# Performance work log

Hardware: AMD Instinct MI355X
Metric: run time of the kernel (lower is better)

Reference implementation:

```python
import jax, jax.numpy as jnp
import numpy as np

N_DAYS, N_HOURS, N_LINKS, N_FEATS = 4, 24, 2000, 4
N_PATHS, N_ODS = 20000, 4000
EPS = 1e-12


def setup_inputs() -> dict:
    key = jax.random.key(0)
    ks = jax.random.split(key, 9)
    # X: (days, hours, links, 1 + n_features); channel 0 is free-flow travel time tt_ff
    X = jax.random.uniform(ks[0], (N_DAYS, N_HOURS, N_LINKS, N_FEATS + 1), dtype=jnp.float32) + 0.1
    # utility coefficients; signs '-' for all cost features (projected via clip to <= 0)
    theta_raw = -jax.random.uniform(ks[1], (N_FEATS,), dtype=jnp.float32)
    theta_links = 0.01 * jax.random.normal(ks[2], (N_LINKS,), dtype=jnp.float32)
    q_sqrt = jax.random.uniform(ks[3], (N_ODS,), dtype=jnp.float32) + 0.5  # q = q_sqrt**2
    log_alpha = 0.1 * jax.random.normal(ks[4], (N_LINKS,), dtype=jnp.float32)
    beta_raw = jax.random.uniform(ks[5], (N_LINKS,), dtype=jnp.float32, minval=1.0, maxval=3.0)
    k = jax.random.uniform(ks[6], (N_LINKS,), dtype=jnp.float32, minval=50.0, maxval=150.0)
    # link-path incidence D (n_links, n_paths), ~10 links per path
    D = (jax.random.uniform(ks[7], (N_LINKS, N_PATHS)) < 0.005).astype(jnp.float32)
    # OD segment id of each path (sorted, one OD per path) == sparse M structure
    od_of_path = jnp.sort(jax.random.randint(ks[8], (N_PATHS,), 0, N_ODS, dtype=jnp.int32))
    return dict(X=X, theta_raw=theta_raw, theta_links=theta_links, q_sqrt=q_sqrt,
                log_alpha=log_alpha, beta_raw=beta_raw, k=k, D=D,
                od_of_path=od_of_path, n_ods=N_ODS)


def reference(X, theta_raw, theta_links, q_sqrt, log_alpha, beta_raw, k, D, od_of_path, n_ods):
    # project_theta: all features have sign '-', so clip to (-inf, 0]
    theta = jnp.minimum(theta_raw, 0.0)
    tt_ff = X[..., 0]              # (d, h, l)
    feats = X[..., 1:]             # (d, h, l, f)
    # link utilities: einsum('ijkl,l->ijk') + theta_links
    V = jnp.einsum('dhlf,f->dhl', feats, theta) + theta_links
    # path utilities: einsum('ijk,kl->ijl') with D (links, paths)
    vf = jnp.einsum('dhl,lp->dhp', V, D)            # (d, h, p)
    vf_t = jnp.moveaxis(vf, -1, 0)                  # (p, d, h) paths leading for segment ops
    # segmented softmax over paths within each OD choice set (sparse M pattern)
    vmax = jax.lax.stop_gradient(
        jax.ops.segment_max(vf_t, od_of_path, num_segments=n_ods))   # (ods, d, h)
    ev = jnp.exp(vf_t - vmax[od_of_path])
    denom = jax.ops.segment_sum(ev, od_of_path, num_segments=n_ods)[od_of_path]
    pf = ev / denom                                  # (p, d, h) path probabilities
    # path flows: pf scaled by OD demand q = q_sqrt**2
    q = q_sqrt ** 2
    f = pf * q[od_of_path][:, None, None]            # (p, d, h)
    # link flows + relu
    x = jax.nn.relu(jnp.einsum('pdh,lp->dhl', f, D))  # (d, h, l)
    # BPR link travel times: tt_ff * (1 + alpha * (x/k)^beta)
    alpha = jnp.exp(log_alpha)
    beta = jnp.clip(beta_raw, EPS, 4.0)
    return tt_ff * (1.0 + alpha * jnp.power(x / k, beta))
```

## Files before the change

kernel.cpp:

```cpp
#include <hip/hip_runtime.h>
#include <math.h>

#define NDH 96
#define ND4 24
#define NL  2000
#define NP  20000
#define NOD 4000
#define PL_CAP 32
#define LP_CAP 150
#define LP_LDS 256

typedef unsigned short u16;
typedef unsigned int   u32;

__global__ __launch_bounds__(256) void kA(const float* __restrict__ X,
                                          const float* __restrict__ theta_raw,
                                          const float* __restrict__ theta_links,
                                          float* __restrict__ V) {
    int gid = blockIdx.x * blockDim.x + threadIdx.x;
    if (gid >= NL * NDH) return;
    int l = gid / NDH, dh = gid - l * NDH;
    float t0 = fminf(theta_raw[0], 0.f);
    float t1 = fminf(theta_raw[1], 0.f);
    float t2 = fminf(theta_raw[2], 0.f);
    float t3 = fminf(theta_raw[3], 0.f);
    const float* xp = X + ((size_t)(dh * NL + l)) * 5;
    V[gid] = theta_links[l]
           + t0 * xp[1] + t1 * xp[2] + t2 * xp[3] + t3 * xp[4];
}

__global__ __launch_bounds__(256) void kB3(const float* __restrict__ D,
                                           int* __restrict__ lc,
                                           u16* __restrict__ lp) {
    __shared__ u16 slp[LP_LDS];
    __shared__ int scnt;
    int l = blockIdx.x;
    int tid = threadIdx.x;
    if (tid == 0) scnt = 0;
    __syncthreads();
    const float4* row4 = (const float4*)(D + (size_t)l * NP);
    for (int i = tid; i < NP / 4; i += 256) {
        float4 fv = row4[i];
        u32 wv[4] = { __float_as_uint(fv.x), __float_as_uint(fv.y),
                      __float_as_uint(fv.z), __float_as_uint(fv.w) };
        if ((wv[0] | wv[1] | wv[2] | wv[3]) == 0u) continue;
        int p0 = i * 4;
#pragma unroll
        for (int k = 0; k < 4; k++) {
            if (wv[k] != 0u) {
                int s = atomicAdd(&scnt, 1);
                if (s < LP_LDS) slp[s] = (u16)(p0 + k);
            }
        }
    }
    __syncthreads();
    int c = min(scnt, LP_CAP);
    for (int j = tid; j < c; j += 256) lp[l * LP_CAP + j] = slp[j];
    if (tid == 0) lc[l] = scnt;
}

__global__ __launch_bounds__(256) void kL2(const int* __restrict__ lc,
                                           const u16* __restrict__ lp,
                                           int* __restrict__ pc,
                                           u16* __restrict__ pl) {
    int t = blockIdx.x * 256 + threadIdx.x;
    int l = t >> 8, j = t & 255;
    if (l >= NL) return;
    if (j >= min(lc[l], LP_CAP)) return;
    int p = (int)lp[l * LP_CAP + j];
    int s = atomicAdd(&pc[p], 1);
    if (s < PL_CAP) pl[p * PL_CAP + s] = (u16)l;
}

__global__ __launch_bounds__(256) void kC(const int* __restrict__ od, int* __restrict__ start) {
    int o = blockIdx.x * blockDim.x + threadIdx.x;
    if (o > NOD) return;
    int lo = 0, hi = NP;
    while (lo < hi) { int mid = (lo + hi) >> 1; if (od[mid] < o) lo = mid + 1; else hi = mid; }
    start[o] = lo;
}

__global__ __launch_bounds__(256) void kD4(const float* __restrict__ V,
                                           const int* __restrict__ pc,
                                           const u16* __restrict__ pl,
                                           float* __restrict__ vf) {
    int tid = blockIdx.x * blockDim.x + threadIdx.x;
    if (tid >= NP * ND4) return;
    int p = tid / ND4, d4 = tid - p * ND4;
    int c = min(pc[p], PL_CAP);
    const u16* plrow = pl + p * PL_CAP;
    const float4* V4 = (const float4*)V;
    float4 acc = make_float4(0.f, 0.f, 0.f, 0.f);
    for (int j0 = 0; j0 < c; j0 += 8) {
        int li[8];
#pragma unroll
        for (int t = 0; t < 8; t++) li[t] = (j0 + t < c) ? (int)plrow[j0 + t] : -1;
#pragma unroll
        for (int t = 0; t < 8; t++) {
            if (li[t] >= 0) {
                float4 v = V4[li[t] * ND4 + d4];
                acc.x += v.x; acc.y += v.y; acc.z += v.z; acc.w += v.w;
            }
        }
    }
    ((float4*)vf)[p * ND4 + d4] = acc;
}

__global__ __launch_bounds__(256) void kE4(float* __restrict__ vf,
                                           const int* __restrict__ start,
                                           const float* __restrict__ q_sqrt) {
    int tid = blockIdx.x * blockDim.x + threadIdx.x;
    if (tid >= NOD * ND4) return;
    int o = tid / ND4, d4 = tid - o * ND4;
    int a = start[o], b = start[o + 1];
    if (a >= b) return;
    float4* vf4 = (float4*)vf;
    float4 m = make_float4(-INFINITY, -INFINITY, -INFINITY, -INFINITY);
    for (int p = a; p < b; p++) {
        float4 v = vf4[p * ND4 + d4];
        m.x = fmaxf(m.x, v.x); m.y = fmaxf(m.y, v.y);
        m.z = fmaxf(m.z, v.z); m.w = fmaxf(m.w, v.w);
    }
    float4 s = make_float4(0.f, 0.f, 0.f, 0.f);
    for (int p = a; p < b; p++) {
        float4 v = vf4[p * ND4 + d4];
        s.x += expf(v.x - m.x); s.y += expf(v.y - m.y);
        s.z += expf(v.z - m.z); s.w += expf(v.w - m.w);
    }
    float q = q_sqrt[o]; float qq = q * q;
    float4 rs = make_float4(qq / s.x, qq / s.y, qq / s.z, qq / s.w);
    for (int p = a; p < b; p++) {
        float4 v = vf4[p * ND4 + d4];
        v.x = expf(v.x - m.x) * rs.x; v.y = expf(v.y - m.y) * rs.y;
        v.z = expf(v.z - m.z) * rs.z; v.w = expf(v.w - m.w) * rs.w;
        vf4[p * ND4 + d4] = v;
    }
}

__global__ __launch_bounds__(192) void kF4(const float* __restrict__ f,
                                           const int* __restrict__ lc,
                                           const u16* __restrict__ lp,
                                           const float* __restrict__ X,
                                           const float* __restrict__ log_alpha,
                                           const float* __restrict__ beta_raw,
                                           const float* __restrict__ kk,
                                           float* __restrict__ out) {
    __shared__ float4 sf[8 * ND4];
    int l  = blockIdx.x;
    int d4 = threadIdx.x % ND4;
    int jc = threadIdx.x / ND4;
    int c  = min(lc[l], LP_CAP);
    const u16* lprow = lp + l * LP_CAP;
    const float4* f4 = (const float4*)f;
    float4 acc = make_float4(0.f, 0.f, 0.f, 0.f);
    for (int j = jc; j < c; j += 8) {
        float4 v = f4[(int)lprow[j] * ND4 + d4];
        acc.x += v.x; acc.y += v.y; acc.z += v.z; acc.w += v.w;
    }
    sf[jc * ND4 + d4] = acc;
    __syncthreads();
    if (jc == 0) {
        float4 t = sf[d4];
#pragma unroll
        for (int r = 1; r < 8; r++) {
            float4 u = sf[r * ND4 + d4];
            t.x += u.x; t.y += u.y; t.z += u.z; t.w += u.w;
        }
        float alpha = expf(log_alpha[l]);
        float beta  = fminf(fmaxf(beta_raw[l], 1e-12f), 4.0f);
        float kv    = kk[l];
        float xs[4] = { t.x, t.y, t.z, t.w };
#pragma unroll
        for (int k4 = 0; k4 < 4; k4++) {
            int dh = d4 * 4 + k4;
            float xv = fmaxf(xs[k4], 0.f);
            float tt = X[((size_t)(dh * NL + l)) * 5];
            out[dh * NL + l] = tt * (1.0f + alpha * powf(xv / kv, beta));
        }
    }
}

extern "C" void kernel_launch(void* const* d_in, const int* in_sizes, int n_in,
                              void* d_out, int out_size, void* d_ws, size_t ws_size,
                              hipStream_t stream) {
    const float* X           = (const float*)d_in[0];
    const float* theta_raw   = (const float*)d_in[1];
    const float* theta_links = (const float*)d_in[2];
    const float* q_sqrt      = (const float*)d_in[3];
    const float* log_alpha   = (const float*)d_in[4];
    const float* beta_raw    = (const float*)d_in[5];
    const float* kk          = (const float*)d_in[6];
    const float* D           = (const float*)d_in[7];
    const int*   od          = (const int*)d_in[8];
    float* out = (float*)d_out;
    char* ws = (char*)d_ws;

    int*   pc    = (int*)(ws + 0);
    int*   lc    = (int*)(ws + 80000);
    int*   start = (int*)(ws + 88064);
    float* V     = (float*)(ws + 104576);
    u16*   pl    = (u16*)(ws + 872576);
    u16*   lp    = (u16*)(ws + 2152576);
    float* vf    = (float*)(ws + 2785024);

    hipMemsetAsync(pc, 0, 80000, stream);

    kA <<<(NL * NDH + 255) / 256, 256, 0, stream>>>(X, theta_raw, theta_links, V);
    kB3<<<NL, 256, 0, stream>>>(D, lc, lp);
    kL2<<<(NL * 256) / 256, 256, 0, stream>>>(lc, lp, pc, pl);
    kC <<<(NOD + 1 + 255) / 256, 256, 0, stream>>>(od, start);
    kD4<<<(NP * ND4 + 255) / 256, 256, 0, stream>>>(V, pc, pl, vf);
    kE4<<<(NOD * ND4 + 255) / 256, 256, 0, stream>>>(vf, start, q_sqrt);
    kF4<<<NL, 192, 0, stream>>>(vf, lc, lp, X, log_alpha, beta_raw, kk, out);
}
```

Baseline: 307.9 us.

## Fuse path-list build into scan kernel and path-utility gather into segmented softmax

The kernel that builds link-to-path lists now also appends each link to its paths' lists, which removes a separate launch. The path-utility gather is fused into the per-OD softmax kernel and recomputed in each of its three passes, so the intermediate vf array is never written to or read from global memory. In exchange the softmax kernel launches only 96k threads instead of 480k, and it repeats the gather three times, so per-thread latency and load imbalance across ODs of different sizes can grow.

```diff
diff --git a/kernel.cpp b/kernel.cpp
--- a/kernel.cpp
+++ b/kernel.cpp
@@ -29,9 +29,11 @@
            + t0 * xp[1] + t1 * xp[2] + t2 * xp[3] + t3 * xp[4];
 }
 
-__global__ __launch_bounds__(256) void kB3(const float* __restrict__ D,
-                                           int* __restrict__ lc,
-                                           u16* __restrict__ lp) {
+__global__ __launch_bounds__(256) void kB3L(const float* __restrict__ D,
+                                            int* __restrict__ lc,
+                                            u16* __restrict__ lp,
+                                            int* __restrict__ pc,
+                                            u16* __restrict__ pl) {
     __shared__ u16 slp[LP_LDS];
     __shared__ int scnt;
     int l = blockIdx.x;
@@ -55,21 +57,13 @@
     }
     __syncthreads();
     int c = min(scnt, LP_CAP);
-    for (int j = tid; j < c; j += 256) lp[l * LP_CAP + j] = slp[j];
+    for (int j = tid; j < c; j += 256) {
+        int p = (int)slp[j];
+        lp[l * LP_CAP + j] = (u16)p;
+        int s = atomicAdd(&pc[p], 1);
+        if (s < PL_CAP) pl[p * PL_CAP + s] = (u16)l;
+    }
     if (tid == 0) lc[l] = scnt;
-}
-
-__global__ __launch_bounds__(256) void kL2(const int* __restrict__ lc,
-                                           const u16* __restrict__ lp,
-                                           int* __restrict__ pc,
-                                           u16* __restrict__ pl) {
-    int t = blockIdx.x * 256 + threadIdx.x;
-    int l = t >> 8, j = t & 255;
-    if (l >= NL) return;
-    if (j >= min(lc[l], LP_CAP)) return;
-    int p = (int)lp[l * LP_CAP + j];
-    int s = atomicAdd(&pc[p], 1);
-    if (s < PL_CAP) pl[p * PL_CAP + s] = (u16)l;
 }
 
 __global__ __launch_bounds__(256) void kC(const int* __restrict__ od, int* __restrict__ start) {
@@ -80,60 +74,76 @@
     start[o] = lo;
 }
 
-__global__ __launch_bounds__(256) void kD4(const float* __restrict__ V,
-                                           const int* __restrict__ pc,
-                                           const u16* __restrict__ pl,
-                                           float* __restrict__ vf) {
-    int tid = blockIdx.x * blockDim.x + threadIdx.x;
-    if (tid >= NP * ND4) return;
-    int p = tid / ND4, d4 = tid - p * ND4;
-    int c = min(pc[p], PL_CAP);
-    const u16* plrow = pl + p * PL_CAP;
-    const float4* V4 = (const float4*)V;
-    float4 acc = make_float4(0.f, 0.f, 0.f, 0.f);
-    for (int j0 = 0; j0 < c; j0 += 8) {
-        int li[8];
-#pragma unroll
-        for (int t = 0; t < 8; t++) li[t] = (j0 + t < c) ? (int)plrow[j0 + t] : -1;
-#pragma unroll
-        for (int t = 0; t < 8; t++) {
-            if (li[t] >= 0) {
-                float4 v = V4[li[t] * ND4 + d4];
-                acc.x += v.x; acc.y += v.y; acc.z += v.z; acc.w += v.w;
-            }
-        }
-    }
-    ((float4*)vf)[p * ND4 + d4] = acc;
-}
-
-__global__ __launch_bounds__(256) void kE4(float* __restrict__ vf,
-                                           const int* __restrict__ start,
-                                           const float* __restrict__ q_sqrt) {
+__global__ __launch_bounds__(256) void kDE4(const float* __restrict__ V,
+                                            const int* __restrict__ start,
+                                            const int* __restrict__ pc,
+                                            const u16* __restrict__ pl,
+                                            const float* __restrict__ q_sqrt,
+                                            float* __restrict__ f) {
     int tid = blockIdx.x * blockDim.x + threadIdx.x;
     if (tid >= NOD * ND4) return;
     int o = tid / ND4, d4 = tid - o * ND4;
     int a = start[o], b = start[o + 1];
     if (a >= b) return;
-    float4* vf4 = (float4*)vf;
+    const float4* V4 = (const float4*)V;
+    float4* f4 = (float4*)f;
+
     float4 m = make_float4(-INFINITY, -INFINITY, -INFINITY, -INFINITY);
     for (int p = a; p < b; p++) {
-        float4 v = vf4[p * ND4 + d4];
-        m.x = fmaxf(m.x, v.x); m.y = fmaxf(m.y, v.y);
-        m.z = fmaxf(m.z, v.z); m.w = fmaxf(m.w, v.w);
+        int c = min(pc[p], PL_CAP);
+        const u16* pr = pl + p * PL_CAP;
+        float4 acc = make_float4(0.f, 0.f, 0.f, 0.f);
+        for (int j0 = 0; j0 < c; j0 += 8) {
+            int li[8];
+#pragma unroll
+            for (int t = 0; t < 8; t++) li[t] = (j0 + t < c) ? (int)pr[j0 + t] : -1;
+#pragma unroll
+            for (int t = 0; t < 8; t++) if (li[t] >= 0) {
+                float4 v = V4[li[t] * ND4 + d4];
+                acc.x += v.x; acc.y += v.y; acc.z += v.z; acc.w += v.w;
+            }
+        }
+        m.x = fmaxf(m.x, acc.x); m.y = fmaxf(m.y, acc.y);
+        m.z = fmaxf(m.z, acc.z); m.w = fmaxf(m.w, acc.w);
     }
     float4 s = make_float4(0.f, 0.f, 0.f, 0.f);
     for (int p = a; p < b; p++) {
-        float4 v = vf4[p * ND4 + d4];
-        s.x += expf(v.x - m.x); s.y += expf(v.y - m.y);
-        s.z += expf(v.z - m.z); s.w += expf(v.w - m.w);
+        int c = min(pc[p], PL_CAP);
+        const u16* pr = pl + p * PL_CAP;
+        float4 acc = make_float4(0.f, 0.f, 0.f, 0.f);
+        for (int j0 = 0; j0 < c; j0 += 8) {
+            int li[8];
+#pragma unroll
+            for (int t = 0; t < 8; t++) li[t] = (j0 + t < c) ? (int)pr[j0 + t] : -1;
+#pragma unroll
+            for (int t = 0; t < 8; t++) if (li[t] >= 0) {
+                float4 v = V4[li[t] * ND4 + d4];
+                acc.x += v.x; acc.y += v.y; acc.z += v.z; acc.w += v.w;
+            }
+        }
+        s.x += expf(acc.x - m.x); s.y += expf(acc.y - m.y);
+        s.z += expf(acc.z - m.z); s.w += expf(acc.w - m.w);
     }
     float q = q_sqrt[o]; float qq = q * q;
     float4 rs = make_float4(qq / s.x, qq / s.y, qq / s.z, qq / s.w);
     for (int p = a; p < b; p++) {
-        float4 v = vf4[p * ND4 + d4];
-        v.x = expf(v.x - m.x) * rs.x; v.y = expf(v.y - m.y) * rs.y;
-        v.z = expf(v.z - m.z) * rs.z; v.w = expf(v.w - m.w) * rs.w;
-        vf4[p * ND4 + d4] = v;
+        int c = min(pc[p], PL_CAP);
+        const u16* pr = pl + p * PL_CAP;
+        float4 acc = make_float4(0.f, 0.f, 0.f, 0.f);
+        for (int j0 = 0; j0 < c; j0 += 8) {
+            int li[8];
+#pragma unroll
+            for (int t = 0; t < 8; t++) li[t] = (j0 + t < c) ? (int)pr[j0 + t] : -1;
+#pragma unroll
+            for (int t = 0; t < 8; t++) if (li[t] >= 0) {
+                float4 v = V4[li[t] * ND4 + d4];
+                acc.x += v.x; acc.y += v.y; acc.z += v.z; acc.w += v.w;
+            }
+        }
+        float4 w;
+        w.x = expf(acc.x - m.x) * rs.x; w.y = expf(acc.y - m.y) * rs.y;
+        w.z = expf(acc.z - m.z) * rs.z; w.w = expf(acc.w - m.w) * rs.w;
+        f4[p * ND4 + d4] = w;
     }
 }
 
@@ -201,15 +211,13 @@
     float* V     = (float*)(ws + 104576);
     u16*   pl    = (u16*)(ws + 872576);
     u16*   lp    = (u16*)(ws + 2152576);
-    float* vf    = (float*)(ws + 2785024);
+    float* f     = (float*)(ws + 2785024);
 
     hipMemsetAsync(pc, 0, 80000, stream);
 
-    kA <<<(NL * NDH + 255) / 256, 256, 0, stream>>>(X, theta_raw, theta_links, V);
-    kB3<<<NL, 256, 0, stream>>>(D, lc, lp);
-    kL2<<<(NL * 256) / 256, 256, 0, stream>>>(lc, lp, pc, pl);
-    kC <<<(NOD + 1 + 255) / 256, 256, 0, stream>>>(od, start);
-    kD4<<<(NP * ND4 + 255) / 256, 256, 0, stream>>>(V, pc, pl, vf);
-    kE4<<<(NOD * ND4 + 255) / 256, 256, 0, stream>>>(vf, start, q_sqrt);
-    kF4<<<NL, 192, 0, stream>>>(vf, lc, lp, X, log_alpha, beta_raw, kk, out);
-}
+    kA  <<<(NL * NDH + 255) / 256, 256, 0, stream>>>(X, theta_raw, theta_links, V);
+    kB3L<<<NL, 256, 0, stream>>>(D, lc, lp, pc, pl);
+    kC  <<<(NOD + 1 + 255) / 256, 256, 0, stream>>>(od, start);
+    kDE4<<<(NOD * ND4 + 255) / 256, 256, 0, stream>>>(V, start, pc, pl, q_sqrt, f);
+    kF4 <<<NL, 192, 0, stream>>>(f, lc, lp, X, log_alpha, beta_raw, kk, out);
+}
```

Measured after the change: 377.2 us. 22.5% more time.
